# Kernel tuning notes

Hardware: AMD Instinct MI355X
Metric: run time of the kernel (lower is better)

## Reference

```python
import jax, jax.numpy as jnp
import numpy as np

B, S, T, D = 16, 512, 16, 128
LN_EPS = 1e-5


def setup_inputs() -> dict:
    key = jax.random.key(0)
    k_x, k_h, k_w = jax.random.split(key, 3)
    x = jax.random.normal(k_x, (B, S, T, D), dtype=jnp.float32)
    # prev_hidden must be strictly positive (code takes its log)
    prev_hidden = jax.random.uniform(k_h, (B, 1, T, D), dtype=jnp.float32) * 0.9 + 0.05
    ln_gamma = jnp.ones((D,), jnp.float32)
    ln_beta = jnp.zeros((D,), jnp.float32)
    # torch Linear(dim, 2*dim): store as (D, 2D) for x @ W
    W = jax.random.normal(k_w, (D, 2 * D), dtype=jnp.float32) * (1.0 / np.sqrt(D))
    b = jnp.zeros((2 * D,), jnp.float32)
    return {"x": x, "prev_hidden": prev_hidden, "ln_gamma": ln_gamma,
            "ln_beta": ln_beta, "W": W, "b": b}


def _g_act_log(h):
    # log of G activation: x>=0 -> log(relu(x)+0.5); x<0 -> -softplus(-x)
    return jnp.where(h >= 0, jnp.log(jax.nn.relu(h) + 0.5), -jax.nn.softplus(-h))


def reference(x, prev_hidden, ln_gamma, ln_beta, W, b):
    seq_len = x.shape[1]
    # LayerNorm over last dim
    mu = jnp.mean(x, axis=-1, keepdims=True)
    var = jnp.var(x, axis=-1, keepdims=True)
    xn = (x - mu) * jax.lax.rsqrt(var + LN_EPS) * ln_gamma + ln_beta
    gh = jnp.einsum('bstd,de->bste', xn, W) + b  # (B,S,T,2D)
    gate, hidden = jnp.split(gh, 2, axis=-1)
    # parallel (seq_len > 1) log-space path
    log_coeffs = -jax.nn.softplus(gate)          # log(1 - z)
    log_z = -jax.nn.softplus(-gate)              # log z
    log_values = log_z + _g_act_log(hidden)      # (B,S,T,D)
    # prepend prev_hidden: values get log(h0), coeffs get zero pad
    log_values = jnp.concatenate([jnp.log(prev_hidden), log_values], axis=1)
    zero_pad = jnp.zeros_like(log_coeffs[:, :1])
    log_coeffs = jnp.concatenate([zero_pad, log_coeffs], axis=1)
    # Heinsen associative scan in log space
    a_star = jnp.cumsum(log_coeffs, axis=1)
    log_h0_plus_b_star = jax.lax.cumlogsumexp(log_values - a_star, axis=1)
    out = jnp.exp(a_star + log_h0_plus_b_star)
    out = out[:, -seq_len:]
    next_prev_hidden = out[:, -1:]
    return out, next_prev_hidden
```

## Files before the change

kernel.cpp:

```cpp
#include <hip/hip_runtime.h>
#include <hip/hip_bf16.h>
#include <stdint.h>

#define BB 16
#define SS 512
#define TT 16
#define DD 128
#define CH 64
#define NCH (SS/CH)
#define LN_EPS 1e-5f

typedef __attribute__((ext_vector_type(8))) short short8;
typedef __attribute__((ext_vector_type(4))) float f32x4;

static __device__ __forceinline__ uint32_t cvt_pk_bf16(float lo, float hi) {
    uint32_t r;
    asm("v_cvt_pk_bf16_f32 %0, %1, %2" : "=v"(r) : "v"(lo), "v"(hi));
    return r;
}

#define BAR() do {                                            \
    asm volatile("s_waitcnt lgkmcnt(0)" ::: "memory");        \
    __builtin_amdgcn_s_barrier();                             \
    asm volatile("" ::: "memory");                            \
} while (0)

__global__ __launch_bounds__(512, 2)
void fused_mingru(
    const float* __restrict__ x, const float* __restrict__ prevh,
    const float* __restrict__ gamma, const float* __restrict__ beta,
    const float* __restrict__ W, const float* __restrict__ bias,
    float* __restrict__ out, float* __restrict__ nexth)
{
    __shared__ __align__(16) unsigned char xnb[2][CH*256];

    const int tid  = threadIdx.x;
    const int w    = tid >> 6;
    const int lane = tid & 63;
    const int l15  = lane & 15;
    const int lhi  = lane >> 4;

    const int bt = blockIdx.x;
    const size_t rowstride = (size_t)TT * DD;
    const size_t base_bt   = ((size_t)(bt >> 4) * SS * TT + (bt & 15)) * DD;

    const int r_ln = tid >> 3;
    const int c8   = tid & 7;
    const int slot_p = ((r_ln >> 2) & 3)*16 + (r_ln >> 4)*4 + (r_ln & 3);
    const int keyx   = slot_p & 7;
    const float* xp0 = x + base_bt + (size_t)r_ln * rowstride + c8*16;

    f32x4 px0, px1, px2, px3;
    auto issuePx = [&](int st) {
        const float* xp = xp0 + (size_t)st * CH * rowstride;
        px0 = *(const f32x4*)(xp + 0);
        px1 = *(const f32x4*)(xp + 4);
        px2 = *(const f32x4*)(xp + 8);
        px3 = *(const f32x4*)(xp + 12);
    };
    issuePx(0);

    short8 wfr[2][4];
    float  bs2[2];
    #pragma unroll
    for (int ni = 0; ni < 2; ++ni) {
        const int col = (ni ? 128 : 0) + w*16 + l15;
        float acc = 0.0f;
        #pragma unroll
        for (int kt = 0; kt < 4; ++kt) {
            union { short8 s8; uint32_t u[4]; } fr;
            #pragma unroll
            for (int p = 0; p < 4; ++p) {
                const int k0 = kt*32 + lhi*8 + 2*p;
                const float w0 = W[(size_t)k0*256 + col];
                const float w1 = W[(size_t)(k0+1)*256 + col];
                acc = fmaf(beta[k0],   w0, acc);
                acc = fmaf(beta[k0+1], w1, acc);
                fr.u[p] = cvt_pk_bf16(gamma[k0]*w0, gamma[k0+1]*w1);
            }
            wfr[ni][kt] = fr.s8;
        }
        acc += __shfl_xor(acc, 16);
        acc += __shfl_xor(acc, 32);
        bs2[ni] = bias[col] + acc;
    }

    float hM = prevh[(size_t)bt*128 + w*16 + l15];

    auto phaseLN = [&](int st) {
        float s1 = px0.x+px0.y+px0.z+px0.w + px1.x+px1.y+px1.z+px1.w
                 + px2.x+px2.y+px2.z+px2.w + px3.x+px3.y+px3.z+px3.w;
        float s2 = px0.x*px0.x+px0.y*px0.y+px0.z*px0.z+px0.w*px0.w
                 + px1.x*px1.x+px1.y*px1.y+px1.z*px1.z+px1.w*px1.w
                 + px2.x*px2.x+px2.y*px2.y+px2.z*px2.z+px2.w*px2.w
                 + px3.x*px3.x+px3.y*px3.y+px3.z*px3.z+px3.w*px3.w;
        s1 += __shfl_xor(s1, 1); s2 += __shfl_xor(s2, 1);
        s1 += __shfl_xor(s1, 2); s2 += __shfl_xor(s2, 2);
        s1 += __shfl_xor(s1, 4); s2 += __shfl_xor(s2, 4);
        const float mu = s1 * (1.0f/128.0f);
        const float rs = rsqrtf(s2 * (1.0f/128.0f) - mu*mu + LN_EPS);
        unsigned char* row = xnb[st & 1] + slot_p*256;
        union { short8 s8; uint32_t u[4]; } a, b2;
        a.u[0]  = cvt_pk_bf16((px0.x-mu)*rs, (px0.y-mu)*rs);
        a.u[1]  = cvt_pk_bf16((px0.z-mu)*rs, (px0.w-mu)*rs);
        a.u[2]  = cvt_pk_bf16((px1.x-mu)*rs, (px1.y-mu)*rs);
        a.u[3]  = cvt_pk_bf16((px1.z-mu)*rs, (px1.w-mu)*rs);
        b2.u[0] = cvt_pk_bf16((px2.x-mu)*rs, (px2.y-mu)*rs);
        b2.u[1] = cvt_pk_bf16((px2.z-mu)*rs, (px2.w-mu)*rs);
        b2.u[2] = cvt_pk_bf16((px3.x-mu)*rs, (px3.y-mu)*rs);
        b2.u[3] = cvt_pk_bf16((px3.z-mu)*rs, (px3.w-mu)*rs);
        *(short8*)(row + (((2*c8)     ^ keyx) << 4)) = a.s8;
        *(short8*)(row + (((2*c8 + 1) ^ keyx) << 4)) = b2.s8;
    };

    auto phaseG = [&](int st) {
        const unsigned char* xb = xnb[st & 1];
        float Cc[16], Cv[16];
        #pragma unroll
        for (int mt = 0; mt < 4; ++mt) {
            const unsigned char* rowp = xb + (mt*16 + l15)*256;
            short8 af[4];
            #pragma unroll
            for (int kt = 0; kt < 4; ++kt) {
                const int c = (kt << 2) | lhi;
                af[kt] = *(const short8*)(rowp + ((c ^ (l15 & 7)) << 4));
            }
            f32x4 ag = (f32x4)(0.f), ah = (f32x4)(0.f);
            #pragma unroll
            for (int kt = 0; kt < 4; ++kt) {
                ag = __builtin_amdgcn_mfma_f32_16x16x32_bf16(af[kt], wfr[0][kt], ag, 0, 0, 0);
                ah = __builtin_amdgcn_mfma_f32_16x16x32_bf16(af[kt], wfr[1][kt], ah, 0, 0, 0);
            }
            #pragma unroll
            for (int j = 0; j < 4; ++j) {
                const float g  = ag[j] + bs2[0];
                const float hh = ah[j] + bs2[1];
                const float cc = 1.0f / (1.0f + __expf(g));
                const float ga = (hh >= 0.0f) ? (hh + 0.5f)
                                              : (1.0f / (1.0f + __expf(-hh)));
                Cc[mt*4 + j] = cc;
                Cv[mt*4 + j] = (1.0f - cc) * ga;
            }
        }
        #pragma unroll
        for (int i = 1; i < 16; ++i) {
            Cv[i] = fmaf(Cc[i], Cv[i-1], Cv[i]);
            Cc[i] = Cc[i] * Cc[i-1];
        }
        float Ic = Cc[15], Iv = Cv[15];
        float pc = __shfl_up(Ic, 16), pv = __shfl_up(Iv, 16);
        if (lhi >= 1) { Iv = fmaf(Ic, pv, Iv); Ic *= pc; }
        pc = __shfl_up(Ic, 32); pv = __shfl_up(Iv, 32);
        if (lhi >= 2) { Iv = fmaf(Ic, pv, Iv); Ic *= pc; }
        float Ec = __shfl_up(Ic, 16), Ev = __shfl_up(Iv, 16);
        if (lhi == 0) { Ec = 1.0f; Ev = 0.0f; }
        const float Mc = __shfl(Ic, 48 + l15);
        const float Mv = __shfl(Iv, 48 + l15);
        const float hE = fmaf(Ec, hM, Ev);
        float* op = out + base_bt + (size_t)(st*CH + lhi*16) * rowstride + w*16 + l15;
        #pragma unroll
        for (int i = 0; i < 16; ++i)
            op[(size_t)i * rowstride] = fmaf(Cc[i], hE, Cv[i]);
        hM = fmaf(Mc, hM, Mv);
    };

    phaseLN(0);
    issuePx(1);
    BAR();

    for (int st = 0; st < NCH; ++st) {
        phaseG(st);
        if (st + 1 < NCH) {
            phaseLN(st + 1);
            if (st + 2 < NCH) issuePx(st + 2);
        }
        BAR();
    }

    if (lane < 16)
        nexth[(size_t)bt*128 + w*16 + lane] = hM;
}

extern "C" void kernel_launch(void* const* d_in, const int* in_sizes, int n_in,
                              void* d_out, int out_size, void* d_ws, size_t ws_size,
                              hipStream_t stream) {
    const float* x     = (const float*)d_in[0];
    const float* prevh = (const float*)d_in[1];
    const float* gamma = (const float*)d_in[2];
    const float* beta  = (const float*)d_in[3];
    const float* W     = (const float*)d_in[4];
    const float* bias  = (const float*)d_in[5];

    float* out   = (float*)d_out;
    float* nexth = out + (size_t)BB*SS*TT*DD;

    fused_mingru<<<BB*TT, 512, 0, stream>>>(x, prevh, gamma, beta, W, bias,
                                            out, nexth);
}
```

Before: 42.35 us.

## Precompute LayerNorm for whole sequence into LDS, then run barrier-free GEMM/scan loop

Replaces the double-buffered per-chunk LN/GEMM interleave with a two-phase schedule. All chunks of the input are normalized into a full-sequence LDS buffer using ping-pong register prefetch, then a single barrier precedes the GEMM and scan loop over all chunks. This removes the per-chunk barriers and coupling between LN and MFMA work. In exchange it uses far more shared memory per block, lowering achievable occupancy, and serializes all loads before any compute or stores.

```diff
diff --git a/kernel.cpp b/kernel.cpp
--- a/kernel.cpp
+++ b/kernel.cpp
@@ -32,7 +32,7 @@
     const float* __restrict__ W, const float* __restrict__ bias,
     float* __restrict__ out, float* __restrict__ nexth)
 {
-    __shared__ __align__(16) unsigned char xnb[2][CH*256];
+    __shared__ __align__(16) unsigned char xnb[SS*256];
 
     const int tid  = threadIdx.x;
     const int w    = tid >> 6;
@@ -50,15 +50,18 @@
     const int keyx   = slot_p & 7;
     const float* xp0 = x + base_bt + (size_t)r_ln * rowstride + c8*16;
 
-    f32x4 px0, px1, px2, px3;
-    auto issuePx = [&](int st) {
-        const float* xp = xp0 + (size_t)st * CH * rowstride;
-        px0 = *(const f32x4*)(xp + 0);
-        px1 = *(const f32x4*)(xp + 4);
-        px2 = *(const f32x4*)(xp + 8);
-        px3 = *(const f32x4*)(xp + 12);
+    f32x4 a0, a1, a2, a3, b0, b1, b2, b3;
+    auto loadA = [&](int ch) {
+        const float* xp = xp0 + (size_t)ch * CH * rowstride;
+        a0 = *(const f32x4*)(xp + 0);  a1 = *(const f32x4*)(xp + 4);
+        a2 = *(const f32x4*)(xp + 8);  a3 = *(const f32x4*)(xp + 12);
     };
-    issuePx(0);
+    auto loadB = [&](int ch) {
+        const float* xp = xp0 + (size_t)ch * CH * rowstride;
+        b0 = *(const f32x4*)(xp + 0);  b1 = *(const f32x4*)(xp + 4);
+        b2 = *(const f32x4*)(xp + 8);  b3 = *(const f32x4*)(xp + 12);
+    };
+    loadA(0);
 
     short8 wfr[2][4];
     float  bs2[2];
@@ -87,34 +90,47 @@
 
     float hM = prevh[(size_t)bt*128 + w*16 + l15];
 
-    auto phaseLN = [&](int st) {
-        float s1 = px0.x+px0.y+px0.z+px0.w + px1.x+px1.y+px1.z+px1.w
-                 + px2.x+px2.y+px2.z+px2.w + px3.x+px3.y+px3.z+px3.w;
-        float s2 = px0.x*px0.x+px0.y*px0.y+px0.z*px0.z+px0.w*px0.w
-                 + px1.x*px1.x+px1.y*px1.y+px1.z*px1.z+px1.w*px1.w
-                 + px2.x*px2.x+px2.y*px2.y+px2.z*px2.z+px2.w*px2.w
-                 + px3.x*px3.x+px3.y*px3.y+px3.z*px3.z+px3.w*px3.w;
+    auto lnStore = [&](int ch, const f32x4& p0, const f32x4& p1,
+                       const f32x4& p2, const f32x4& p3) {
+        float s1 = p0.x+p0.y+p0.z+p0.w + p1.x+p1.y+p1.z+p1.w
+                 + p2.x+p2.y+p2.z+p2.w + p3.x+p3.y+p3.z+p3.w;
+        float s2 = p0.x*p0.x+p0.y*p0.y+p0.z*p0.z+p0.w*p0.w
+                 + p1.x*p1.x+p1.y*p1.y+p1.z*p1.z+p1.w*p1.w
+                 + p2.x*p2.x+p2.y*p2.y+p2.z*p2.z+p2.w*p2.w
+                 + p3.x*p3.x+p3.y*p3.y+p3.z*p3.z+p3.w*p3.w;
         s1 += __shfl_xor(s1, 1); s2 += __shfl_xor(s2, 1);
         s1 += __shfl_xor(s1, 2); s2 += __shfl_xor(s2, 2);
         s1 += __shfl_xor(s1, 4); s2 += __shfl_xor(s2, 4);
         const float mu = s1 * (1.0f/128.0f);
         const float rs = rsqrtf(s2 * (1.0f/128.0f) - mu*mu + LN_EPS);
-        unsigned char* row = xnb[st & 1] + slot_p*256;
-        union { short8 s8; uint32_t u[4]; } a, b2;
-        a.u[0]  = cvt_pk_bf16((px0.x-mu)*rs, (px0.y-mu)*rs);
-        a.u[1]  = cvt_pk_bf16((px0.z-mu)*rs, (px0.w-mu)*rs);
-        a.u[2]  = cvt_pk_bf16((px1.x-mu)*rs, (px1.y-mu)*rs);
-        a.u[3]  = cvt_pk_bf16((px1.z-mu)*rs, (px1.w-mu)*rs);
-        b2.u[0] = cvt_pk_bf16((px2.x-mu)*rs, (px2.y-mu)*rs);
-        b2.u[1] = cvt_pk_bf16((px2.z-mu)*rs, (px2.w-mu)*rs);
-        b2.u[2] = cvt_pk_bf16((px3.x-mu)*rs, (px3.y-mu)*rs);
-        b2.u[3] = cvt_pk_bf16((px3.z-mu)*rs, (px3.w-mu)*rs);
+        unsigned char* row = xnb + (ch*CH + slot_p)*256;
+        union { short8 s8; uint32_t u[4]; } a, b;
+        a.u[0] = cvt_pk_bf16((p0.x-mu)*rs, (p0.y-mu)*rs);
+        a.u[1] = cvt_pk_bf16((p0.z-mu)*rs, (p0.w-mu)*rs);
+        a.u[2] = cvt_pk_bf16((p1.x-mu)*rs, (p1.y-mu)*rs);
+        a.u[3] = cvt_pk_bf16((p1.z-mu)*rs, (p1.w-mu)*rs);
+        b.u[0] = cvt_pk_bf16((p2.x-mu)*rs, (p2.y-mu)*rs);
+        b.u[1] = cvt_pk_bf16((p2.z-mu)*rs, (p2.w-mu)*rs);
+        b.u[2] = cvt_pk_bf16((p3.x-mu)*rs, (p3.y-mu)*rs);
+        b.u[3] = cvt_pk_bf16((p3.z-mu)*rs, (p3.w-mu)*rs);
         *(short8*)(row + (((2*c8)     ^ keyx) << 4)) = a.s8;
-        *(short8*)(row + (((2*c8 + 1) ^ keyx) << 4)) = b2.s8;
+        *(short8*)(row + (((2*c8 + 1) ^ keyx) << 4)) = b.s8;
     };
 
-    auto phaseG = [&](int st) {
-        const unsigned char* xb = xnb[st & 1];
+    #pragma unroll
+    for (int ch = 0; ch < NCH; ++ch) {
+        if ((ch & 1) == 0) {
+            if (ch + 1 < NCH) loadB(ch + 1);
+            lnStore(ch, a0, a1, a2, a3);
+        } else {
+            if (ch + 1 < NCH) loadA(ch + 1);
+            lnStore(ch, b0, b1, b2, b3);
+        }
+    }
+    BAR();
+
+    for (int st = 0; st < NCH; ++st) {
+        const unsigned char* xb = xnb + st*CH*256;
         float Cc[16], Cv[16];
         #pragma unroll
         for (int mt = 0; mt < 4; ++mt) {
@@ -162,19 +178,6 @@
         for (int i = 0; i < 16; ++i)
             op[(size_t)i * rowstride] = fmaf(Cc[i], hE, Cv[i]);
         hM = fmaf(Mc, hM, Mv);
-    };
-
-    phaseLN(0);
-    issuePx(1);
-    BAR();
-
-    for (int st = 0; st < NCH; ++st) {
-        phaseG(st);
-        if (st + 1 < NCH) {
-            phaseLN(st + 1);
-            if (st + 2 < NCH) issuePx(st + 2);
-        }
-        BAR();
     }
 
     if (lane < 16)
```

Measured after the change: 44.74 us. 5.6% more time.
